# Optimization experiments

Hardware: AMD Instinct MI355X
Metric: run time of the kernel (lower is better)

The kernel has to match this reference:

```python
import jax, jax.numpy as jnp
import numpy as np

EPS = 1e-9
THRESHOLD = 0.2          # second_policy_eval = 'threshold'
CAP_FACTOR = 2.0         # capacity_factor_eval
MIN_EXPERT_CAPACITY = 4


def setup_inputs() -> dict:
    key = jax.random.key(0)
    k1, k2 = jax.random.split(key)
    x = jax.random.normal(k1, (8, 2048, 1024), dtype=jnp.float32)
    W = jax.random.normal(k2, (1024, 64), dtype=jnp.float32) * 0.02
    return {"x": x, "W": W}


def _cumsum_exclusive(t):
    # exclusive cumsum along token dim (-2)
    return jnp.cumsum(t, axis=-2) - t


def reference(x, W):
    b, n, d = x.shape
    e = W.shape[1]
    dt = x.dtype

    raw_gates = jax.nn.softmax(jnp.einsum('bnd,de->bne', x, W), axis=-1)  # [b,n,e]

    gate_1 = jnp.max(raw_gates, axis=-1)            # [b,n]
    index_1 = jnp.argmax(raw_gates, axis=-1)        # [b,n]
    mask_1 = jax.nn.one_hot(index_1, e, dtype=dt)   # [b,n,e]
    density_1_proxy = raw_gates

    gates_wo_top1 = raw_gates * (1.0 - mask_1)
    gate_2 = jnp.max(gates_wo_top1, axis=-1)
    index_2 = jnp.argmax(gates_wo_top1, axis=-1)
    mask_2 = jax.nn.one_hot(index_2, e, dtype=dt)

    denom = gate_1 + gate_2 + EPS
    gate_1 = gate_1 / denom
    gate_2 = gate_2 / denom

    density_1 = jnp.mean(mask_1, axis=-2)                         # [b,e]
    density_1_proxy_m = jnp.mean(density_1_proxy, axis=-2)        # [b,e]
    loss = jnp.mean(density_1_proxy_m * density_1) * float(e ** 2)

    # policy == 'threshold'
    mask_2 = mask_2 * (gate_2 > THRESHOLD).astype(dt)[..., None]

    expert_capacity = max(min(n, int(n * CAP_FACTOR / e)), MIN_EXPERT_CAPACITY)
    cap_f = float(expert_capacity)

    position_in_expert_1 = _cumsum_exclusive(mask_1) * mask_1
    mask_1 = mask_1 * (position_in_expert_1 < cap_f).astype(dt)
    mask_1_count = jnp.sum(mask_1, axis=-2, keepdims=True)        # [b,1,e]
    mask_1_flat = jnp.sum(mask_1, axis=-1)                        # [b,n]
    position_in_expert_1 = jnp.sum(position_in_expert_1, axis=-1) # [b,n]
    gate_1 = gate_1 * mask_1_flat

    position_in_expert_2 = _cumsum_exclusive(mask_2) + mask_1_count
    position_in_expert_2 = position_in_expert_2 * mask_2
    mask_2 = mask_2 * (position_in_expert_2 < cap_f).astype(dt)
    mask_2_flat = jnp.sum(mask_2, axis=-1)
    position_in_expert_2 = jnp.sum(position_in_expert_2, axis=-1)
    gate_2 = gate_2 * mask_2_flat

    # combine: [b, n, e, capacity]
    oh_e1 = jax.nn.one_hot(index_1, e, dtype=dt)[..., None]                                    # [b,n,e,1]
    oh_c1 = jax.nn.one_hot(position_in_expert_1.astype(jnp.int32), expert_capacity, dtype=dt)[..., None, :]  # [b,n,1,cap]
    oh_e2 = jax.nn.one_hot(index_2, e, dtype=dt)[..., None]
    oh_c2 = jax.nn.one_hot(position_in_expert_2.astype(jnp.int32), expert_capacity, dtype=dt)[..., None, :]

    combine_tensor = (
        (gate_1 * mask_1_flat)[..., None, None] * oh_e1 * oh_c1
        + (gate_2 * mask_2_flat)[..., None, None] * oh_e2 * oh_c2
    )
    dispatch_tensor = (combine_tensor != 0).astype(dt)
    return dispatch_tensor, combine_tensor, loss
```

## Files before the change

kernel.cpp:

```cpp
#include <hip/hip_runtime.h>
#include <math.h>

#define BB 8
#define NN 2048
#define DD 1024
#define EE 64
#define CAP 64
#define NTOK (BB * NN)
#define OUT_T_FLOATS 67108864
#define OUT_T_F4     16777216


__global__ __launch_bounds__(256) void gating_kernel(
    const float* __restrict__ x, const float* __restrict__ W,
    float4* __restrict__ recs, float* __restrict__ dens)
{
    __shared__ float Wl[64 * 64];
    __shared__ float dred[4][64];

    const int lane = threadIdx.x & 63;
    const int wave = __builtin_amdgcn_readfirstlane(threadIdx.x >> 6);
    const int tok0 = blockIdx.x * 32 + wave * 8;
    const float* xr = x + (size_t)tok0 * DD;

    float acc[8];
#pragma unroll
    for (int t = 0; t < 8; ++t) acc[t] = 0.f;

    for (int dc = 0; dc < 16; ++dc) {
        __syncthreads();
        {
            const float4* wg = (const float4*)(W + dc * 64 * 64);
            float4* wl = (float4*)Wl;
#pragma unroll
            for (int k = 0; k < 4; ++k)
                wl[threadIdx.x + 256 * k] = wg[threadIdx.x + 256 * k];
        }
        __syncthreads();
        const float* xc = xr + dc * 64;
#pragma unroll 8
        for (int dd = 0; dd < 64; ++dd) {
            float w = Wl[dd * 64 + lane];
#pragma unroll
            for (int t = 0; t < 8; ++t)
                acc[t] = fmaf(xc[(size_t)t * DD + dd], w, acc[t]);
        }
    }

    float densacc = 0.f;
#pragma unroll 1
    for (int t = 0; t < 8; ++t) {
        const float lv = acc[t];
        float v = lv; int bi = lane;
#pragma unroll
        for (int off = 32; off; off >>= 1) {
            float ov = __shfl_xor(v, off);
            int   oi = __shfl_xor(bi, off);
            if (ov > v || (ov == v && oi < bi)) { v = ov; bi = oi; }
        }
        const float m1 = v; const int i1 = bi;
        float v2 = (lane == i1) ? -INFINITY : lv; int b2 = lane;
#pragma unroll
        for (int off = 32; off; off >>= 1) {
            float ov = __shfl_xor(v2, off);
            int   oi = __shfl_xor(b2, off);
            if (ov > v2 || (ov == v2 && oi < b2)) { v2 = ov; b2 = oi; }
        }
        const float m2 = v2; const int i2 = b2;

        float ex = expf(lv - m1);
        float Z = ex;
#pragma unroll
        for (int off = 32; off; off >>= 1) Z += __shfl_xor(Z, off);
        float g1 = 1.0f / Z;
        float g2 = expf(m2 - m1) * g1;
        float den = g1 + g2 + 1e-9f;
        float g1n = g1 / den;
        float g2n = g2 / den;
        int flag = (g2n > 0.2f) ? 1 : 0;

        densacc += ex * g1;

        if (lane == 0)
            recs[tok0 + t] = make_float4(g1n, g2n, __int_as_float(i1),
                                         __int_as_float(i2 | (flag << 8)));
    }

    dred[wave][lane] = densacc;
    __syncthreads();
    if (wave == 0) {
        float s = dred[0][lane] + dred[1][lane] + dred[2][lane] + dred[3][lane];
        dens[blockIdx.x * 64 + lane] = s;
    }
}

__global__ __launch_bounds__(1024) void scan_kernel(
    const float4* __restrict__ recs, const float* __restrict__ dens,
    float4* __restrict__ frecs, float* __restrict__ lossp)
{
    const int b = blockIdx.x;
    __shared__ short i1s[NN], i2s[NN];
    __shared__ unsigned char fls[NN];
    __shared__ short p1loc[NN], p2loc[NN];
    __shared__ int hist1[16][64], pre1[16][64], hist2[16][64], pre2[16][64];
    __shared__ int base2[64], total1[64];
    __shared__ float dsum[64];

    const int tid = threadIdx.x;
    const int lane = tid & 63;
    const int wave = tid >> 6;

    for (int i = tid; i < NN; i += 1024) {
        float4 r = recs[b * NN + i];
        int i1  = __float_as_int(r.z);
        int i2f = __float_as_int(r.w);
        i1s[i] = (short)i1;
        i2s[i] = (short)(i2f & 63);
        fls[i] = (unsigned char)(i2f >> 8);
        p2loc[i] = 0;
    }
    if (tid < 64) {
        float s = 0.f;
        for (int k = 0; k < 64; ++k) s += dens[(b * 64 + k) * 64 + tid];
        dsum[tid] = s;
    }
    __syncthreads();

    {
        const int base = wave * 128;
        int cnt = 0;
        for (int i = 0; i < 128; ++i) {
            int e1 = i1s[base + i];
            if (lane == e1) { p1loc[base + i] = (short)cnt; ++cnt; }
        }
        hist1[wave][lane] = cnt;
        int cnt2 = 0;
        for (int i = 0; i < 128; ++i) {
            int ok = fls[base + i];
            int e2 = i2s[base + i];
            if (ok && lane == e2) { p2loc[base + i] = (short)cnt2; ++cnt2; }
        }
        hist2[wave][lane] = cnt2;
    }
    __syncthreads();

    if (wave == 0) {
        int run = 0;
#pragma unroll
        for (int w = 0; w < 16; ++w) { pre1[w][lane] = run; run += hist1[w][lane]; }
        total1[lane] = run;
        base2[lane] = run < CAP ? run : CAP;
        int run2 = 0;
#pragma unroll
        for (int w = 0; w < 16; ++w) { pre2[w][lane] = run2; run2 += hist2[w][lane]; }
        float v = dsum[lane] * (float)run;
#pragma unroll
        for (int off = 32; off; off >>= 1) v += __shfl_xor(v, off);
        if (lane == 0) lossp[b] = v;
    }
    __syncthreads();

    for (int i = tid; i < NN; i += 1024) {
        int w = i >> 7;
        float4 r = recs[b * NN + i];
        int e1 = i1s[i];
        int p1 = (int)p1loc[i] + pre1[w][e1];
        int k1 = p1 < CAP;
        int e2 = i2s[i];
        int fl = fls[i];
        int p2 = (int)p2loc[i] + pre2[w][e2] + base2[e2];
        int k2 = fl && (p2 < CAP);
        float4 fr;
        fr.x = k1 ? r.x : 0.f;
        fr.y = k2 ? r.y : 0.f;
        fr.z = __int_as_float(k1 ? (e1 * CAP + p1) : -1);
        fr.w = __int_as_float(k2 ? (e2 * CAP + p2) : -1);
        frecs[b * NN + i] = fr;
    }
}

__global__ __launch_bounds__(256) void fill_kernel(
    const float4* __restrict__ frecs, const float* __restrict__ lossp,
    float* __restrict__ out)
{
    const int tid = blockIdx.x * 256 + threadIdx.x;
    const int token = tid >> 10;
    const int e  = (tid >> 4) & 63;
    const int c4 = tid & 15;
    float4 r = frecs[token];

    float cx = 0.f, cy = 0.f, cz = 0.f, cw = 0.f;
    float dx = 0.f, dy = 0.f, dz = 0.f, dw = 0.f;

    int p1 = __float_as_int(r.z);
    if (p1 >= 0 && (p1 >> 6) == e && ((p1 >> 2) & 15) == c4) {
        int cc = p1 & 3;
        if      (cc == 0) { cx = r.x; dx = 1.f; }
        else if (cc == 1) { cy = r.x; dy = 1.f; }
        else if (cc == 2) { cz = r.x; dz = 1.f; }
        else              { cw = r.x; dw = 1.f; }
    }
    int p2 = __float_as_int(r.w);
    if (p2 >= 0 && (p2 >> 6) == e && ((p2 >> 2) & 15) == c4) {
        int cc = p2 & 3;
        if      (cc == 0) { cx = r.y; dx = 1.f; }
        else if (cc == 1) { cy = r.y; dy = 1.f; }
        else if (cc == 2) { cz = r.y; dz = 1.f; }
        else              { cw = r.y; dw = 1.f; }
    }

    float4* o4 = (float4*)out;
    o4[tid]             = make_float4(dx, dy, dz, dw);
    o4[tid + OUT_T_F4]  = make_float4(cx, cy, cz, cw);

    if (tid == 0) {
        float s = 0.f;
        for (int k = 0; k < 8; ++k) s += lossp[k];
        out[2 * OUT_T_FLOATS] = s * (1.0f / 524288.0f);
    }
}

extern "C" void kernel_launch(void* const* d_in, const int* in_sizes, int n_in,
                              void* d_out, int out_size, void* d_ws, size_t ws_size,
                              hipStream_t stream)
{
    const float* x = (const float*)d_in[0];
    const float* W = (const float*)d_in[1];
    float* out = (float*)d_out;
    char* ws = (char*)d_ws;

    float4* recs  = (float4*)(ws);
    float4* frecs = (float4*)(ws + 262144);
    float*  dens  = (float*)(ws + 524288);
    float*  lossp = (float*)(ws + 655360);

    gating_kernel<<<512, 256, 0, stream>>>(x, W, recs, dens);
    scan_kernel<<<8, 1024, 0, stream>>>(recs, dens, frecs, lossp);
    fill_kernel<<<65536, 256, 0, stream>>>(frecs, lossp, out);
}
```

Baseline: 682.2 us.

## Vectorize gating loads, ballot-based scan ranks, wider nontemporal fill stores

The gating GEMV now reads x as float4 and applies four W rows per load, which cuts scalar global load instructions. The scan replaces its serial per-lane loops over shared arrays with wave ballot and popcount ranking in 64-token groups, so the shared staging arrays go away. The fill kernel has each thread write 8 floats with nontemporal stores for both outputs and launches half as many blocks, aiming to speed up the dominant 512 MB output write. Risks are a different store pattern, and the ballot logic must reproduce the reference tie-breaking order.

```diff
diff --git a/kernel.cpp b/kernel.cpp
--- a/kernel.cpp
+++ b/kernel.cpp
@@ -10,6 +10,8 @@
 #define OUT_T_FLOATS 67108864
 #define OUT_T_F4     16777216
 
+typedef float vfloat4 __attribute__((ext_vector_type(4)));
+
 
 __global__ __launch_bounds__(256) void gating_kernel(
     const float* __restrict__ x, const float* __restrict__ W,
@@ -21,7 +23,6 @@
     const int lane = threadIdx.x & 63;
     const int wave = __builtin_amdgcn_readfirstlane(threadIdx.x >> 6);
     const int tok0 = blockIdx.x * 32 + wave * 8;
-    const float* xr = x + (size_t)tok0 * DD;
 
     float acc[8];
 #pragma unroll
@@ -37,13 +38,21 @@
                 wl[threadIdx.x + 256 * k] = wg[threadIdx.x + 256 * k];
         }
         __syncthreads();
-        const float* xc = xr + dc * 64;
-#pragma unroll 8
-        for (int dd = 0; dd < 64; ++dd) {
-            float w = Wl[dd * 64 + lane];
-#pragma unroll
-            for (int t = 0; t < 8; ++t)
-                acc[t] = fmaf(xc[(size_t)t * DD + dd], w, acc[t]);
+        const float4* xc4 = (const float4*)(x + (size_t)tok0 * DD + dc * 64);
+#pragma unroll 2
+        for (int q = 0; q < 16; ++q) {
+            const float w0 = Wl[(q * 4 + 0) * 64 + lane];
+            const float w1 = Wl[(q * 4 + 1) * 64 + lane];
+            const float w2 = Wl[(q * 4 + 2) * 64 + lane];
+            const float w3 = Wl[(q * 4 + 3) * 64 + lane];
+#pragma unroll
+            for (int t = 0; t < 8; ++t) {
+                const float4 xv = xc4[t * 256 + q];
+                acc[t] = fmaf(xv.x, w0, acc[t]);
+                acc[t] = fmaf(xv.y, w1, acc[t]);
+                acc[t] = fmaf(xv.z, w2, acc[t]);
+                acc[t] = fmaf(xv.w, w3, acc[t]);
+            }
         }
     }
 
@@ -99,60 +108,67 @@
     float4* __restrict__ frecs, float* __restrict__ lossp)
 {
     const int b = blockIdx.x;
-    __shared__ short i1s[NN], i2s[NN];
-    __shared__ unsigned char fls[NN];
-    __shared__ short p1loc[NN], p2loc[NN];
-    __shared__ int hist1[16][64], pre1[16][64], hist2[16][64], pre2[16][64];
-    __shared__ int base2[64], total1[64];
+    __shared__ int hist1[32][64], pre1[32][64];
+    __shared__ int hist2[32][64], pre2[32][64];
+    __shared__ int base2[64];
     __shared__ float dsum[64];
 
     const int tid = threadIdx.x;
     const int lane = tid & 63;
     const int wave = tid >> 6;
 
-    for (int i = tid; i < NN; i += 1024) {
-        float4 r = recs[b * NN + i];
-        int i1  = __float_as_int(r.z);
-        int i2f = __float_as_int(r.w);
-        i1s[i] = (short)i1;
-        i2s[i] = (short)(i2f & 63);
-        fls[i] = (unsigned char)(i2f >> 8);
-        p2loc[i] = 0;
-    }
-    if (tid < 64) {
+    float4 r[2];
+    int e1[2], e2[2], fl[2], rank1[2], rank2[2];
+    const unsigned long long below = (1ull << lane) - 1ull;
+
+#pragma unroll
+    for (int u = 0; u < 2; ++u) {
+        const int g = 2 * wave + u;
+        const int tok = g * 64 + lane;
+        float4 rr = recs[b * NN + tok];
+        r[u] = rr;
+        e1[u] = __float_as_int(rr.z);
+        int i2f = __float_as_int(rr.w);
+        e2[u] = i2f & 63;
+        fl[u] = i2f >> 8;
+
+        unsigned long long m = ~0ull, mv = ~0ull;
+#pragma unroll
+        for (int bit = 0; bit < 6; ++bit) {
+            unsigned long long vt = __ballot((e1[u] >> bit) & 1);
+            m  &= ((e1[u] >> bit) & 1) ? vt : ~vt;
+            mv &= ((lane  >> bit) & 1) ? vt : ~vt;
+        }
+        rank1[u] = __popcll(m & below);
+        hist1[g][lane] = __popcll(mv);
+
+        unsigned long long fv = __ballot(fl[u]);
+        m = fv; mv = fv;
+#pragma unroll
+        for (int bit = 0; bit < 6; ++bit) {
+            unsigned long long vt = __ballot((e2[u] >> bit) & 1);
+            m  &= ((e2[u] >> bit) & 1) ? vt : ~vt;
+            mv &= ((lane  >> bit) & 1) ? vt : ~vt;
+        }
+        rank2[u] = __popcll(m & below);
+        hist2[g][lane] = __popcll(mv);
+    }
+
+    if (wave == 0) {
         float s = 0.f;
-        for (int k = 0; k < 64; ++k) s += dens[(b * 64 + k) * 64 + tid];
-        dsum[tid] = s;
-    }
-    __syncthreads();
-
-    {
-        const int base = wave * 128;
-        int cnt = 0;
-        for (int i = 0; i < 128; ++i) {
-            int e1 = i1s[base + i];
-            if (lane == e1) { p1loc[base + i] = (short)cnt; ++cnt; }
-        }
-        hist1[wave][lane] = cnt;
-        int cnt2 = 0;
-        for (int i = 0; i < 128; ++i) {
-            int ok = fls[base + i];
-            int e2 = i2s[base + i];
-            if (ok && lane == e2) { p2loc[base + i] = (short)cnt2; ++cnt2; }
-        }
-        hist2[wave][lane] = cnt2;
+        for (int k = 0; k < 64; ++k) s += dens[(b * 64 + k) * 64 + lane];
+        dsum[lane] = s;
     }
     __syncthreads();
 
     if (wave == 0) {
         int run = 0;
 #pragma unroll
-        for (int w = 0; w < 16; ++w) { pre1[w][lane] = run; run += hist1[w][lane]; }
-        total1[lane] = run;
+        for (int g = 0; g < 32; ++g) { pre1[g][lane] = run; run += hist1[g][lane]; }
         base2[lane] = run < CAP ? run : CAP;
         int run2 = 0;
 #pragma unroll
-        for (int w = 0; w < 16; ++w) { pre2[w][lane] = run2; run2 += hist2[w][lane]; }
+        for (int g = 0; g < 32; ++g) { pre2[g][lane] = run2; run2 += hist2[g][lane]; }
         float v = dsum[lane] * (float)run;
 #pragma unroll
         for (int off = 32; off; off >>= 1) v += __shfl_xor(v, off);
@@ -160,22 +176,20 @@
     }
     __syncthreads();
 
-    for (int i = tid; i < NN; i += 1024) {
-        int w = i >> 7;
-        float4 r = recs[b * NN + i];
-        int e1 = i1s[i];
-        int p1 = (int)p1loc[i] + pre1[w][e1];
+#pragma unroll
+    for (int u = 0; u < 2; ++u) {
+        const int g = 2 * wave + u;
+        const int tok = g * 64 + lane;
+        int p1 = rank1[u] + pre1[g][e1[u]];
         int k1 = p1 < CAP;
-        int e2 = i2s[i];
-        int fl = fls[i];
-        int p2 = (int)p2loc[i] + pre2[w][e2] + base2[e2];
-        int k2 = fl && (p2 < CAP);
+        int p2 = rank2[u] + pre2[g][e2[u]] + base2[e2[u]];
+        int k2 = fl[u] && (p2 < CAP);
         float4 fr;
-        fr.x = k1 ? r.x : 0.f;
-        fr.y = k2 ? r.y : 0.f;
-        fr.z = __int_as_float(k1 ? (e1 * CAP + p1) : -1);
-        fr.w = __int_as_float(k2 ? (e2 * CAP + p2) : -1);
-        frecs[b * NN + i] = fr;
+        fr.x = k1 ? r[u].x : 0.f;
+        fr.y = k2 ? r[u].y : 0.f;
+        fr.z = __int_as_float(k1 ? (e1[u] * CAP + p1) : -1);
+        fr.w = __int_as_float(k2 ? (e2[u] * CAP + p2) : -1);
+        frecs[b * NN + tok] = fr;
     }
 }
 
@@ -184,34 +198,35 @@
     float* __restrict__ out)
 {
     const int tid = blockIdx.x * 256 + threadIdx.x;
-    const int token = tid >> 10;
-    const int e  = (tid >> 4) & 63;
-    const int c4 = tid & 15;
-    float4 r = frecs[token];
-
-    float cx = 0.f, cy = 0.f, cz = 0.f, cw = 0.f;
-    float dx = 0.f, dy = 0.f, dz = 0.f, dw = 0.f;
-
-    int p1 = __float_as_int(r.z);
-    if (p1 >= 0 && (p1 >> 6) == e && ((p1 >> 2) & 15) == c4) {
-        int cc = p1 & 3;
-        if      (cc == 0) { cx = r.x; dx = 1.f; }
-        else if (cc == 1) { cy = r.x; dy = 1.f; }
-        else if (cc == 2) { cz = r.x; dz = 1.f; }
-        else              { cw = r.x; dw = 1.f; }
-    }
-    int p2 = __float_as_int(r.w);
-    if (p2 >= 0 && (p2 >> 6) == e && ((p2 >> 2) & 15) == c4) {
-        int cc = p2 & 3;
-        if      (cc == 0) { cx = r.y; dx = 1.f; }
-        else if (cc == 1) { cy = r.y; dy = 1.f; }
-        else if (cc == 2) { cz = r.y; dz = 1.f; }
-        else              { cw = r.y; dw = 1.f; }
-    }
-
-    float4* o4 = (float4*)out;
-    o4[tid]             = make_float4(dx, dy, dz, dw);
-    o4[tid + OUT_T_F4]  = make_float4(cx, cy, cz, cw);
+    const int token = tid >> 9;
+    const int e  = (tid >> 3) & 63;
+    const int c8 = tid & 7;
+    const float4 r = frecs[token];
+
+    const int p1 = __float_as_int(r.z);
+    const int p2 = __float_as_int(r.w);
+    const int s0 = e * 64 + c8 * 8;
+
+    float dv[8], cv[8];
+#pragma unroll
+    for (int j = 0; j < 8; ++j) {
+        const int s = s0 + j;
+        const bool h1 = (p1 == s);
+        const bool h2 = (p2 == s);
+        dv[j] = (h1 | h2) ? 1.f : 0.f;
+        cv[j] = h1 ? r.x : (h2 ? r.y : 0.f);
+    }
+
+    vfloat4* o4 = (vfloat4*)out;
+    const size_t o = (size_t)tid * 2;
+    vfloat4 d0 = {dv[0], dv[1], dv[2], dv[3]};
+    vfloat4 d1 = {dv[4], dv[5], dv[6], dv[7]};
+    vfloat4 c0 = {cv[0], cv[1], cv[2], cv[3]};
+    vfloat4 c1 = {cv[4], cv[5], cv[6], cv[7]};
+    __builtin_nontemporal_store(d0, o4 + o);
+    __builtin_nontemporal_store(d1, o4 + o + 1);
+    __builtin_nontemporal_store(c0, o4 + OUT_T_F4 + o);
+    __builtin_nontemporal_store(c1, o4 + OUT_T_F4 + o + 1);
 
     if (tid == 0) {
         float s = 0.f;
@@ -236,5 +251,5 @@
 
     gating_kernel<<<512, 256, 0, stream>>>(x, W, recs, dens);
     scan_kernel<<<8, 1024, 0, stream>>>(recs, dens, frecs, lossp);
-    fill_kernel<<<65536, 256, 0, stream>>>(frecs, lossp, out);
-}
+    fill_kernel<<<32768, 256, 0, stream>>>(frecs, lossp, out);
+}
```

New measurement: 803.2 us. +17.7%, slower.
